# Optimization experiments

Hardware: AMD Instinct MI355X
Metric: run time of the kernel (lower is better)

The kernel has to match this reference:

```python
import jax, jax.numpy as jnp
import numpy as np

STATE_DIM = 256
ACTION_DIM = 2
HIDDEN = 512
N_HEADS = 5          # per ensemble; 2*N_HEADS stacked critics total
CEM_POP = 4096
CEM_ITERS = 4
ELITE_N = max(1, int(round(CEM_POP * 0.2)))  # 819
ACTION_LOW, ACTION_HIGH = -1.0, 1.0
INIT_STD, MIN_STD = 0.4, 0.1


def setup_inputs() -> dict:
    key = jax.random.key(0)
    ks = jax.random.split(key, 6)
    in_dim = STATE_DIM + ACTION_DIM
    state = jax.random.normal(ks[0], (1, STATE_DIM), dtype=jnp.float32)
    noise = jax.random.normal(ks[1], (CEM_ITERS, CEM_POP, ACTION_DIM), dtype=jnp.float32)
    W1 = jax.random.normal(ks[2], (2 * N_HEADS, in_dim, HIDDEN), dtype=jnp.float32) / np.sqrt(in_dim).astype(np.float32)
    b1 = jnp.zeros((2 * N_HEADS, HIDDEN), dtype=jnp.float32)
    W2 = jax.random.normal(ks[3], (2 * N_HEADS, HIDDEN, HIDDEN), dtype=jnp.float32) / np.sqrt(HIDDEN).astype(np.float32)
    b2 = jnp.zeros((2 * N_HEADS, HIDDEN), dtype=jnp.float32)
    W3 = jax.random.normal(ks[4], (2 * N_HEADS, HIDDEN, 1), dtype=jnp.float32) / np.sqrt(HIDDEN).astype(np.float32)
    b3 = jnp.zeros((2 * N_HEADS, 1), dtype=jnp.float32)
    return {"state": state, "noise": noise, "W1": W1, "b1": b1, "W2": W2, "b2": b2, "W3": W3, "b3": b3}


def _ensemble_scores(s_batch, a, W1, b1, W2, b2, W3, b3):
    # x: [P, state+action]; heads stacked on leading dim h = 2*N_HEADS
    x = jnp.concatenate([s_batch, a], axis=-1)
    h = jax.nn.relu(jnp.einsum('pi,hij->hpj', x, W1) + b1[:, None, :])
    h = jax.nn.relu(jnp.einsum('hpj,hjk->hpk', h, W2) + b2[:, None, :])
    q = (jnp.einsum('hpk,hko->hpo', h, W3) + b3[:, None, :])[..., 0]  # [2H, P]
    q1, q2 = q[:N_HEADS], q[N_HEADS:]
    return jnp.minimum(q1, q2).mean(axis=0)  # [P]


def reference(state, noise, W1, b1, W2, b2, W3, b3):
    s = state[0]  # squeeze(0)
    s_batch = jnp.broadcast_to(s, (CEM_POP, STATE_DIM))

    def step(carry, eps):
        mu, std, best_a, best_score = carry
        a = jnp.clip(mu + std * eps, ACTION_LOW, ACTION_HIGH)  # [P, A]
        scores = _ensemble_scores(s_batch, a, W1, b1, W2, b2, W3, b3)
        vals, idx = jax.lax.top_k(scores, ELITE_N)
        elite = a[idx]  # [ELITE_N, A]
        mu2 = elite.mean(axis=0)
        std2 = jnp.maximum(jnp.std(elite, axis=0, ddof=1), MIN_STD)  # torch unbiased std
        better = vals[0] > best_score
        best_a2 = jnp.where(better, elite[0], best_a)
        best_score2 = jnp.where(better, vals[0], best_score)
        return (mu2, std2, best_a2, best_score2), None

    carry0 = (jnp.zeros((ACTION_DIM,), jnp.float32),
              jnp.full((ACTION_DIM,), INIT_STD, jnp.float32),
              jnp.zeros((ACTION_DIM,), jnp.float32),
              jnp.float32(-jnp.inf))
    (mu, std, best_a, best_score), _ = jax.lax.scan(step, carry0, noise)
    return best_a[None, :]  # [1, ACTION_DIM]
```

## Files before the change

### kernel.cpp

```cpp
#include <hip/hip_runtime.h>
#include <math.h>

#define SDIM   256
#define HID    512
#define NH     5
#define HEADS  10
#define POP    4096
#define ITERS  4
#define ELITE  819
#define INIT_STDF 0.4f
#define MIN_STDF  0.1f

#define WS_BASE1 0
#define WS_Q     5120
#define WS_STATE 87040
#define WS_W2S_BYTE 348224
#define W2S_USHORTS (HEADS * 2 * 16 * 16384)
#define WS_NEED_BYTES (WS_W2S_BYTE + (size_t)W2S_USHORTS * 2)

typedef __attribute__((ext_vector_type(4))) float f32x4;
typedef __attribute__((ext_vector_type(8))) short bf16x8;

static __device__ __forceinline__ unsigned short bf16_rne(float x) {
    unsigned b = __float_as_uint(x);
    return (unsigned short)((b + 0x7FFFu + ((b >> 16) & 1u)) >> 16);
}

static __device__ __forceinline__ unsigned pack2(float x, float y) {
    unsigned r;
    asm("v_cvt_pk_bf16_f32 %0, %1, %2" : "=v"(r) : "v"(x), "v"(y));
    return r;
}

__global__ __launch_bounds__(256) void k_base(const float* __restrict__ state,
                                              const float* __restrict__ W1,
                                              const float* __restrict__ b1,
                                              float* __restrict__ ws)
{
    const int h = blockIdx.y;
    const int j = blockIdx.x * 256 + threadIdx.x;
    const float* w1h = W1 + (size_t)h * 258 * HID;
    float acc = b1[h * HID + j];
    for (int i = 0; i < SDIM; ++i)
        acc += state[i] * w1h[(size_t)i * HID + j];
    ws[WS_BASE1 + h * HID + j] = acc;

    if (h == 0 && blockIdx.x == 0 && threadIdx.x == 0) {
        float* st = ws + WS_STATE;
        st[0] = 0.f; st[1] = 0.f;
        st[2] = INIT_STDF; st[3] = INIT_STDF;
        st[4] = 0.f; st[5] = 0.f;
        st[6] = -3.402823466e38f;
    }
}

__global__ __launch_bounds__(256) void k_split(const float* __restrict__ W2,
                                               unsigned short* __restrict__ W2S)
{
    const int h = blockIdx.z, cb = blockIdx.y, jc = blockIdx.x;
    const int c = threadIdx.x;
    unsigned short* slab = W2S + (size_t)((h * 2 + cb) * 16 + jc) * 16384;
    #pragma unroll
    for (int jg = 0; jg < 4; ++jg) {
        unsigned hp[4], lp[4];
        #pragma unroll
        for (int i = 0; i < 4; ++i) {
            const int j = jc * 32 + jg * 8 + 2 * i;
            float v0 = W2[(size_t)(h * HID + j) * HID + cb * 256 + c];
            float v1 = W2[(size_t)(h * HID + j + 1) * HID + cb * 256 + c];
            unsigned short h0 = bf16_rne(v0), h1 = bf16_rne(v1);
            float f0 = __uint_as_float((unsigned)h0 << 16);
            float f1 = __uint_as_float((unsigned)h1 << 16);
            unsigned short l0 = bf16_rne(v0 - f0), l1 = bf16_rne(v1 - f1);
            hp[i] = (unsigned)h0 | ((unsigned)h1 << 16);
            lp[i] = (unsigned)l0 | ((unsigned)l1 << 16);
        }
        uint4 HV, LV;
        HV.x = hp[0]; HV.y = hp[1]; HV.z = hp[2]; HV.w = hp[3];
        LV.x = lp[0]; LV.y = lp[1]; LV.z = lp[2]; LV.w = lp[3];
        *(uint4*)&slab[jg * 2048 + c * 8] = HV;
        *(uint4*)&slab[8192 + jg * 2048 + c * 8] = LV;
    }
}

__global__ __launch_bounds__(256, 2) void k_score_mfma4(
    const float* __restrict__ noise, const float* __restrict__ W1,
    const unsigned short* __restrict__ W2S,
    const float* __restrict__ b2, const float* __restrict__ W3,
    float* __restrict__ ws, int t)
{
    __shared__ unsigned short As[2][8192];
    __shared__ float red[4][128];

    const int tid = threadIdx.x;
    const int bid = blockIdx.x;
    const int w = (bid & 7) * 80 + (bid >> 3);
    const int h = w >> 6;
    const int rem = w & 63;
    const int cb = rem >> 5;
    const int rb = rem & 31;

    const int lane = tid & 63;
    const int wc = tid >> 6;
    const int l15 = lane & 15, lk = lane >> 4;

    const int arow = tid & 127;
    const int khalf = tid >> 7;
    const float* st = ws + WS_STATE;
    float2 e = *(const float2*)&noise[((size_t)t * POP + rb * 128 + arow) * 2];
    const float a0 = fminf(fmaxf(st[0] + st[2] * e.x, -1.f), 1.f);
    const float a1 = fminf(fmaxf(st[1] + st[3] * e.y, -1.f), 1.f);

    const float* base1 = ws + WS_BASE1 + h * HID;
    const float* w1u = W1 + ((size_t)h * 258 + 256) * HID;
    const float* w1v = W1 + ((size_t)h * 258 + 257) * HID;
    const unsigned short* bslab = W2S + (size_t)((h * 2 + cb) * 16) * 16384;

    auto computeA = [&](int jc, int buf) {
        #pragma unroll
        for (int g = 0; g < 2; ++g) {
            const int j = jc * 32 + khalf * 16 + g * 8;
            f32x4 b0 = *(const f32x4*)&base1[j];
            f32x4 b1v = *(const f32x4*)&base1[j + 4];
            f32x4 u0 = *(const f32x4*)&w1u[j];
            f32x4 u1 = *(const f32x4*)&w1u[j + 4];
            f32x4 v0 = *(const f32x4*)&w1v[j];
            f32x4 v1 = *(const f32x4*)&w1v[j + 4];
            float hv[8];
            #pragma unroll
            for (int i = 0; i < 4; ++i) {
                hv[i]     = fmaxf(b0[i] + a0 * u0[i] + a1 * v0[i], 0.f);
                hv[4 + i] = fmaxf(b1v[i] + a0 * u1[i] + a1 * v1[i], 0.f);
            }
            unsigned ph[4], pl[4];
            #pragma unroll
            for (int i = 0; i < 4; ++i) {
                ph[i] = pack2(hv[2 * i], hv[2 * i + 1]);
                float fx = __uint_as_float(ph[i] << 16);
                float fy = __uint_as_float(ph[i] & 0xFFFF0000u);
                pl[i] = pack2(hv[2 * i] - fx, hv[2 * i + 1] - fy);
            }
            uint4 HV, LV;
            HV.x = ph[0]; HV.y = ph[1]; HV.z = ph[2]; HV.w = ph[3];
            LV.x = pl[0]; LV.y = pl[1]; LV.z = pl[2]; LV.w = pl[3];
            const int kg = khalf * 2 + g;
            *(uint4*)&As[buf][(kg * 128 + arow) * 8] = HV;
            *(uint4*)&As[buf][4096 + (kg * 128 + arow) * 8] = LV;
        }
    };

    const int bco = (wc * 64 + l15) * 8 + lk * 2048;

    f32x4 acc[8][4];
    #pragma unroll
    for (int m = 0; m < 8; ++m)
        #pragma unroll
        for (int n = 0; n < 4; ++n)
            acc[m][n] = (f32x4){0.f, 0.f, 0.f, 0.f};

    bf16x8 cBH[4], nBH[4], BL[4];
    computeA(0, 0);
    #pragma unroll
    for (int n = 0; n < 4; ++n)
        cBH[n] = *(const bf16x8*)(bslab + bco + n * 128);
    __syncthreads();

    for (int tt = 0; tt < 16; ++tt) {
        const int cur = tt & 1;
        const size_t chunk = (size_t)tt * 16384;
        #pragma unroll
        for (int n = 0; n < 4; ++n)
            BL[n] = *(const bf16x8*)(bslab + chunk + 8192 + bco + n * 128);
        if (tt < 15) {
            #pragma unroll
            for (int n = 0; n < 4; ++n)
                nBH[n] = *(const bf16x8*)(bslab + chunk + 16384 + bco + n * 128);
            computeA(tt + 1, cur ^ 1);
        }
        #pragma unroll
        for (int mg = 0; mg < 2; ++mg) {
            const int abase = (lk * 128 + mg * 64 + l15) * 8;
            bf16x8 AH[4], AL[4];
            #pragma unroll
            for (int m4 = 0; m4 < 4; ++m4) {
                AH[m4] = *(const bf16x8*)&As[cur][abase + m4 * 128];
                AL[m4] = *(const bf16x8*)&As[cur][4096 + abase + m4 * 128];
            }
            #pragma unroll
            for (int m4 = 0; m4 < 4; ++m4)
                #pragma unroll
                for (int n = 0; n < 4; ++n)
                    acc[mg * 4 + m4][n] = __builtin_amdgcn_mfma_f32_16x16x32_bf16(
                        AH[m4], cBH[n], acc[mg * 4 + m4][n], 0, 0, 0);
            #pragma unroll
            for (int m4 = 0; m4 < 4; ++m4)
                #pragma unroll
                for (int n = 0; n < 4; ++n)
                    acc[mg * 4 + m4][n] = __builtin_amdgcn_mfma_f32_16x16x32_bf16(
                        AL[m4], cBH[n], acc[mg * 4 + m4][n], 0, 0, 0);
            #pragma unroll
            for (int m4 = 0; m4 < 4; ++m4)
                #pragma unroll
                for (int n = 0; n < 4; ++n)
                    acc[mg * 4 + m4][n] = __builtin_amdgcn_mfma_f32_16x16x32_bf16(
                        AH[m4], BL[n], acc[mg * 4 + m4][n], 0, 0, 0);
        }
        __syncthreads();
        #pragma unroll
        for (int n = 0; n < 4; ++n) cBH[n] = nBH[n];
    }

    float qp[8][4];
    #pragma unroll
    for (int m = 0; m < 8; ++m)
        #pragma unroll
        for (int r = 0; r < 4; ++r) qp[m][r] = 0.f;
    #pragma unroll
    for (int n = 0; n < 4; ++n) {
        int gcol = cb * 256 + wc * 64 + n * 16 + l15;
        float b2v = b2[h * HID + gcol];
        float w3v = W3[h * HID + gcol];
        #pragma unroll
        for (int m = 0; m < 8; ++m)
            #pragma unroll
            for (int r = 0; r < 4; ++r)
                qp[m][r] += fmaxf(acc[m][n][r] + b2v, 0.f) * w3v;
    }
    #pragma unroll
    for (int m = 0; m < 8; ++m)
        #pragma unroll
        for (int r = 0; r < 4; ++r) {
            float v = qp[m][r];
            v += __shfl_xor(v, 1);
            v += __shfl_xor(v, 2);
            v += __shfl_xor(v, 4);
            v += __shfl_xor(v, 8);
            if (l15 == 0) red[wc][m * 16 + lk * 4 + r] = v;
        }
    __syncthreads();
    if (tid < 128) {
        float q = red[0][tid] + red[1][tid] + red[2][tid] + red[3][tid];
        ws[WS_Q + (size_t)(cb * HEADS + h) * POP + rb * 128 + tid] = q;
    }
}

__global__ __launch_bounds__(256) void k_score(const float* __restrict__ noise,
                                               const float* __restrict__ W1,
                                               const float* __restrict__ W2,
                                               const float* __restrict__ b2,
                                               const float* __restrict__ W3,
                                               float* __restrict__ ws, int t)
{
    __shared__ float h1[32][HID];
    __shared__ float a0s[32], a1s[32];
    __shared__ float red[2][16][2];

    const int tid = threadIdx.x;
    const int h   = blockIdx.y;
    const int p0  = blockIdx.x * 32;

    if (tid < 32) {
        const float* st = ws + WS_STATE;
        const int p = p0 + tid;
        float e0 = noise[((size_t)t * POP + p) * 2 + 0];
        float e1 = noise[((size_t)t * POP + p) * 2 + 1];
        a0s[tid] = fminf(fmaxf(st[0] + st[2] * e0, -1.f), 1.f);
        a1s[tid] = fminf(fmaxf(st[1] + st[3] * e1, -1.f), 1.f);
    }
    __syncthreads();

    const float* base1 = ws + WS_BASE1 + h * HID;
    const float* w1u = W1 + ((size_t)h * 258 + 256) * HID;
    const float* w1v = W1 + ((size_t)h * 258 + 257) * HID;
    #pragma unroll
    for (int jj = 0; jj < 2; ++jj) {
        int j = tid + jj * 256;
        float bb = base1[j], uu = w1u[j], vv = w1v[j];
        #pragma unroll
        for (int p = 0; p < 32; ++p)
            h1[p][j] = fmaxf(bb + a0s[p] * uu + a1s[p] * vv, 0.f);
    }
    __syncthreads();

    const int pg = tid >> 7;
    const int kl = tid & 127;
    const float* W2h = W2 + (size_t)h * HID * HID + kl;

    float acc[16][4];
    #pragma unroll
    for (int p = 0; p < 16; ++p)
        #pragma unroll
        for (int dk = 0; dk < 4; ++dk) acc[p][dk] = 0.f;

    for (int j0 = 0; j0 < HID; j0 += 4) {
        float w[4][4];
        #pragma unroll
        for (int dj = 0; dj < 4; ++dj)
            #pragma unroll
            for (int dk = 0; dk < 4; ++dk)
                w[dj][dk] = W2h[(size_t)(j0 + dj) * HID + dk * 128];
        #pragma unroll
        for (int p = 0; p < 16; ++p) {
            const float4 hv = *(const float4*)&h1[pg * 16 + p][j0];
            #pragma unroll
            for (int dk = 0; dk < 4; ++dk)
                acc[p][dk] += hv.x * w[0][dk] + hv.y * w[1][dk]
                            + hv.z * w[2][dk] + hv.w * w[3][dk];
        }
    }

    float b2v[4], w3v[4];
    #pragma unroll
    for (int dk = 0; dk < 4; ++dk) {
        b2v[dk] = b2[h * HID + kl + dk * 128];
        w3v[dk] = W3[h * HID + kl + dk * 128];
    }
    const int wid  = tid >> 6;
    const int lane = tid & 63;
    const int wig  = wid & 1;
    #pragma unroll
    for (int p = 0; p < 16; ++p) {
        float v = 0.f;
        #pragma unroll
        for (int dk = 0; dk < 4; ++dk)
            v += fmaxf(acc[p][dk] + b2v[dk], 0.f) * w3v[dk];
        #pragma unroll
        for (int off = 32; off; off >>= 1) v += __shfl_down(v, off);
        if (lane == 0) red[pg][p][wig] = v;
    }
    __syncthreads();
    if (tid < 32) {
        int pp = tid & 15, g = tid >> 4;
        ws[WS_Q + (size_t)h * POP + p0 + g * 16 + pp] =
            red[g][pp][0] + red[g][pp][1];
        ws[WS_Q + (size_t)(HEADS + h) * POP + p0 + g * 16 + pp] = 0.f;
    }
}

__global__ __launch_bounds__(256) void k_select(const float* __restrict__ noise,
                                                const float* __restrict__ b3,
                                                float* __restrict__ ws,
                                                float* __restrict__ out, int t)
{
    __shared__ float    sc[POP];
    __shared__ unsigned uk[POP];
    __shared__ unsigned hist[256];
    __shared__ int      scan[256];
    __shared__ float    rf[256];
    __shared__ int      ri_[256];
    __shared__ double   rd[256];
    __shared__ unsigned s_prefix;
    __shared__ int      s_r;

    const int tid = threadIdx.x;
    const float* q = ws + WS_Q;
    float* st = ws + WS_STATE;
    const float mu0 = st[0], mu1 = st[1], sd0 = st[2], sd1 = st[3];

    #pragma unroll
    for (int g = 0; g < 4; ++g) {
        const int p = g * 1024 + tid * 4;
        f32x4 s = (f32x4){0.f, 0.f, 0.f, 0.f};
        #pragma unroll
        for (int hh = 0; hh < NH; ++hh) {
            f32x4 qa0 = *(const f32x4*)&q[(size_t)hh * POP + p];
            f32x4 qa1 = *(const f32x4*)&q[(size_t)(HEADS + hh) * POP + p];
            f32x4 qb0 = *(const f32x4*)&q[(size_t)(NH + hh) * POP + p];
            f32x4 qb1 = *(const f32x4*)&q[(size_t)(HEADS + NH + hh) * POP + p];
            float ba = b3[hh], bb = b3[NH + hh];
            #pragma unroll
            for (int i = 0; i < 4; ++i)
                s[i] += fminf(qa0[i] + qa1[i] + ba, qb0[i] + qb1[i] + bb);
        }
        #pragma unroll
        for (int i = 0; i < 4; ++i) {
            float v = s[i] * 0.2f;
            sc[p + i] = v;
            unsigned b = __float_as_uint(v);
            uk[p + i] = (b & 0x80000000u) ? ~b : (b | 0x80000000u);
        }
    }
    __syncthreads();

    float mv = -3.402823466e38f; int mi = 0;
    for (int p = tid; p < POP; p += 256) {
        float v = sc[p];
        if (v > mv) { mv = v; mi = p; }
    }
    rf[tid] = mv; ri_[tid] = mi;
    __syncthreads();
    for (int off = 128; off; off >>= 1) {
        if (tid < off) {
            float ov = rf[tid + off]; int oi = ri_[tid + off];
            if (ov > rf[tid] || (ov == rf[tid] && oi < ri_[tid])) {
                rf[tid] = ov; ri_[tid] = oi;
            }
        }
        __syncthreads();
    }
    const float maxsc = rf[0];
    const int argmax = ri_[0];
    __syncthreads();

    unsigned prefix = 0; int r = ELITE;
    for (int shift = 24; shift >= 0; shift -= 8) {
        hist[tid] = 0;
        __syncthreads();
        const unsigned himask = (shift < 24) ? (0xFFFFFFFFu << (shift + 8)) : 0u;
        for (int p = tid; p < POP; p += 256) {
            unsigned key = uk[p];
            if ((key & himask) == prefix)
                atomicAdd(&hist[(key >> shift) & 255u], 1u);
        }
        __syncthreads();
        scan[tid] = (int)hist[tid];
        __syncthreads();
        for (int off = 1; off < 256; off <<= 1) {
            int v = (tid + off < 256) ? scan[tid + off] : 0;
            __syncthreads();
            scan[tid] += v;
            __syncthreads();
        }
        int above = (tid < 255) ? scan[tid + 1] : 0;
        if (scan[tid] >= r && above < r) {
            s_prefix = prefix | ((unsigned)tid << shift);
            s_r = r - above;
        }
        __syncthreads();
        prefix = s_prefix; r = s_r;
        __syncthreads();
    }
    const unsigned uT = prefix;
    const int take = r;

    int tieloc = 0;
    {
        const int base = tid * 16;
        #pragma unroll
        for (int k = 0; k < 16; ++k) if (uk[base + k] == uT) tieloc++;
    }
    scan[tid] = tieloc;
    __syncthreads();
    for (int off = 1; off < 256; off <<= 1) {
        int v = (tid >= off) ? scan[tid - off] : 0;
        __syncthreads();
        scan[tid] += v;
        __syncthreads();
    }
    const int tieExcl = scan[tid] - tieloc;

    double s0 = 0, s1 = 0, ss0 = 0, ss1 = 0;
    {
        const int base = tid * 16;
        int trank = tieExcl;
        for (int k = 0; k < 16; ++k) {
            const int p = base + k;
            const unsigned key = uk[p];
            bool inc = false;
            if (key > uT) inc = true;
            else if (key == uT) { if (trank < take) inc = true; trank++; }
            if (inc) {
                float e0 = noise[((size_t)t * POP + p) * 2 + 0];
                float e1 = noise[((size_t)t * POP + p) * 2 + 1];
                float a0 = fminf(fmaxf(mu0 + sd0 * e0, -1.f), 1.f);
                float a1 = fminf(fmaxf(mu1 + sd1 * e1, -1.f), 1.f);
                s0 += a0; s1 += a1;
                ss0 += (double)a0 * a0; ss1 += (double)a1 * a1;
            }
        }
    }
    double S0, S1, SS0, SS1;
    rd[tid] = s0;  __syncthreads();
    for (int off = 128; off; off >>= 1) { if (tid < off) rd[tid] += rd[tid + off]; __syncthreads(); }
    S0 = rd[0]; __syncthreads();
    rd[tid] = s1;  __syncthreads();
    for (int off = 128; off; off >>= 1) { if (tid < off) rd[tid] += rd[tid + off]; __syncthreads(); }
    S1 = rd[0]; __syncthreads();
    rd[tid] = ss0; __syncthreads();
    for (int off = 128; off; off >>= 1) { if (tid < off) rd[tid] += rd[tid + off]; __syncthreads(); }
    SS0 = rd[0]; __syncthreads();
    rd[tid] = ss1; __syncthreads();
    for (int off = 128; off; off >>= 1) { if (tid < off) rd[tid] += rd[tid + off]; __syncthreads(); }
    SS1 = rd[0]; __syncthreads();

    if (tid == 0) {
        const double n = (double)ELITE;
        double m0 = S0 / n, m1 = S1 / n;
        double v0 = (SS0 - S0 * S0 / n) / (n - 1.0);
        double v1 = (SS1 - S1 * S1 / n) / (n - 1.0);
        float nsd0 = fmaxf((float)sqrt(fmax(v0, 0.0)), MIN_STDF);
        float nsd1 = fmaxf((float)sqrt(fmax(v1, 0.0)), MIN_STDF);
        float e0 = noise[((size_t)t * POP + argmax) * 2 + 0];
        float e1 = noise[((size_t)t * POP + argmax) * 2 + 1];
        float a0 = fminf(fmaxf(mu0 + sd0 * e0, -1.f), 1.f);
        float a1 = fminf(fmaxf(mu1 + sd1 * e1, -1.f), 1.f);
        if (maxsc > st[6]) { st[4] = a0; st[5] = a1; st[6] = maxsc; }
        st[0] = (float)m0; st[1] = (float)m1; st[2] = nsd0; st[3] = nsd1;
        if (t == ITERS - 1) { out[0] = st[4]; out[1] = st[5]; }
    }
}

extern "C" void kernel_launch(void* const* d_in, const int* in_sizes, int n_in,
                              void* d_out, int out_size, void* d_ws, size_t ws_size,
                              hipStream_t stream)
{
    const float* state = (const float*)d_in[0];
    const float* noise = (const float*)d_in[1];
    const float* W1    = (const float*)d_in[2];
    const float* b1    = (const float*)d_in[3];
    const float* W2    = (const float*)d_in[4];
    const float* b2    = (const float*)d_in[5];
    const float* W3    = (const float*)d_in[6];
    const float* b3    = (const float*)d_in[7];
    float* out = (float*)d_out;
    float* ws  = (float*)d_ws;

    const bool fast = ws_size >= WS_NEED_BYTES;

    k_base<<<dim3(2, HEADS), 256, 0, stream>>>(state, W1, b1, ws);
    if (fast) {
        unsigned short* W2S = (unsigned short*)((char*)d_ws + WS_W2S_BYTE);
        k_split<<<dim3(16, 2, HEADS), 256, 0, stream>>>(W2, W2S);
        for (int t = 0; t < ITERS; ++t) {
            k_score_mfma4<<<dim3(640), 256, 0, stream>>>(
                noise, W1, W2S, b2, W3, ws, t);
            k_select<<<1, 256, 0, stream>>>(noise, b3, ws, out, t);
        }
    } else {
        for (int t = 0; t < ITERS; ++t) {
            k_score<<<dim3(POP / 32, HEADS), 256, 0, stream>>>(noise, W1, W2, b2, W3, ws, t);
            k_select<<<1, 256, 0, stream>>>(noise, b3, ws, out, t);
        }
    }
}
```

Measured before the change: 368.9 us.

## Build layer-1 activations in registers, drop LDS staging, halve row tile

The score kernel no longer stages layer-1 hidden activations in shared memory. Each wave computes its own A fragments (hi and lo bf16 split) directly in registers, so the per-chunk __syncthreads is removed. The row tile per block drops from 128 to 64, which doubles the grid to 1280 blocks and halves the accumulator registers. Layer-1 weight vectors are prefetched one chunk ahead, and s_setprio raises priority around the MFMA bursts. The cost is that all four waves now compute the same A fragments redundantly, and each B fragment is reused over half as many rows, which doubles B traffic from L2.

After: 400.6 us. 8.6% more time.

```diff
diff --git a/kernel.cpp b/kernel.cpp
--- a/kernel.cpp
+++ b/kernel.cpp
@@ -30,6 +30,17 @@
     unsigned r;
     asm("v_cvt_pk_bf16_f32 %0, %1, %2" : "=v"(r) : "v"(x), "v"(y));
     return r;
+}
+
+static __device__ __forceinline__ bf16x8 mk8(unsigned p0, unsigned p1,
+                                             unsigned p2, unsigned p3) {
+    union { unsigned u[4]; bf16x8 v; } c;
+    c.u[0] = p0; c.u[1] = p1; c.u[2] = p2; c.u[3] = p3;
+    return c.v;
+}
+
+static __device__ __forceinline__ float clip1(float x) {
+    return fminf(fmaxf(x, -1.f), 1.f);
 }
 
 __global__ __launch_bounds__(256) void k_base(const float* __restrict__ state,
@@ -83,54 +94,88 @@
     }
 }
 
-__global__ __launch_bounds__(256, 2) void k_score_mfma4(
+__global__ __launch_bounds__(256, 2) void k_score_mfma5(
     const float* __restrict__ noise, const float* __restrict__ W1,
     const unsigned short* __restrict__ W2S,
     const float* __restrict__ b2, const float* __restrict__ W3,
     float* __restrict__ ws, int t)
 {
-    __shared__ unsigned short As[2][8192];
-    __shared__ float red[4][128];
+    __shared__ float red[4][64];
 
     const int tid = threadIdx.x;
     const int bid = blockIdx.x;
-    const int w = (bid & 7) * 80 + (bid >> 3);
-    const int h = w >> 6;
-    const int rem = w & 63;
-    const int cb = rem >> 5;
-    const int rb = rem & 31;
+    const int w = (bid & 7) * 160 + (bid >> 3);
+    const int h = w >> 7;
+    const int rem = w & 127;
+    const int cb = rem >> 6;
+    const int rs = rem & 63;
 
     const int lane = tid & 63;
-    const int wc = tid >> 6;
+    const int wv = tid >> 6;
     const int l15 = lane & 15, lk = lane >> 4;
 
-    const int arow = tid & 127;
-    const int khalf = tid >> 7;
     const float* st = ws + WS_STATE;
-    float2 e = *(const float2*)&noise[((size_t)t * POP + rb * 128 + arow) * 2];
-    const float a0 = fminf(fmaxf(st[0] + st[2] * e.x, -1.f), 1.f);
-    const float a1 = fminf(fmaxf(st[1] + st[3] * e.y, -1.f), 1.f);
+    const float mu0 = st[0], mu1 = st[1], sd0 = st[2], sd1 = st[3];
+    float a0[4], a1[4];
+    #pragma unroll
+    for (int m = 0; m < 4; ++m) {
+        int r = rs * 64 + m * 16 + l15;
+        float2 e = *(const float2*)&noise[((size_t)t * POP + r) * 2];
+        a0[m] = clip1(mu0 + sd0 * e.x);
+        a1[m] = clip1(mu1 + sd1 * e.y);
+    }
 
     const float* base1 = ws + WS_BASE1 + h * HID;
     const float* w1u = W1 + ((size_t)h * 258 + 256) * HID;
     const float* w1v = W1 + ((size_t)h * 258 + 257) * HID;
     const unsigned short* bslab = W2S + (size_t)((h * 2 + cb) * 16) * 16384;
-
-    auto computeA = [&](int jc, int buf) {
-        #pragma unroll
-        for (int g = 0; g < 2; ++g) {
-            const int j = jc * 32 + khalf * 16 + g * 8;
-            f32x4 b0 = *(const f32x4*)&base1[j];
-            f32x4 b1v = *(const f32x4*)&base1[j + 4];
-            f32x4 u0 = *(const f32x4*)&w1u[j];
-            f32x4 u1 = *(const f32x4*)&w1u[j + 4];
-            f32x4 v0 = *(const f32x4*)&w1v[j];
-            f32x4 v1 = *(const f32x4*)&w1v[j + 4];
+    const int bco = lk * 2048 + (wv * 64 + l15) * 8;
+
+    f32x4 acc[4][4];
+    #pragma unroll
+    for (int m = 0; m < 4; ++m)
+        #pragma unroll
+        for (int n = 0; n < 4; ++n)
+            acc[m][n] = (f32x4){0.f, 0.f, 0.f, 0.f};
+
+    f32x4 pb0 = *(const f32x4*)&base1[lk * 8];
+    f32x4 pb1 = *(const f32x4*)&base1[lk * 8 + 4];
+    f32x4 pu0 = *(const f32x4*)&w1u[lk * 8];
+    f32x4 pu1 = *(const f32x4*)&w1u[lk * 8 + 4];
+    f32x4 pv0 = *(const f32x4*)&w1v[lk * 8];
+    f32x4 pv1 = *(const f32x4*)&w1v[lk * 8 + 4];
+    bf16x8 BH[4];
+    #pragma unroll
+    for (int n = 0; n < 4; ++n)
+        BH[n] = *(const bf16x8*)(bslab + bco + n * 128);
+
+    for (int kc = 0; kc < 16; ++kc) {
+        const size_t ch = (size_t)kc * 16384;
+        bf16x8 BL[4], nBH[4];
+        #pragma unroll
+        for (int n = 0; n < 4; ++n)
+            BL[n] = *(const bf16x8*)(bslab + ch + 8192 + bco + n * 128);
+        f32x4 qb0, qb1, qu0, qu1, qv0, qv1;
+        if (kc < 15) {
+            #pragma unroll
+            for (int n = 0; n < 4; ++n)
+                nBH[n] = *(const bf16x8*)(bslab + ch + 16384 + bco + n * 128);
+            const int j = (kc + 1) * 32 + lk * 8;
+            qb0 = *(const f32x4*)&base1[j];
+            qb1 = *(const f32x4*)&base1[j + 4];
+            qu0 = *(const f32x4*)&w1u[j];
+            qu1 = *(const f32x4*)&w1u[j + 4];
+            qv0 = *(const f32x4*)&w1v[j];
+            qv1 = *(const f32x4*)&w1v[j + 4];
+        }
+        bf16x8 AH[4], AL[4];
+        #pragma unroll
+        for (int m = 0; m < 4; ++m) {
             float hv[8];
             #pragma unroll
             for (int i = 0; i < 4; ++i) {
-                hv[i]     = fmaxf(b0[i] + a0 * u0[i] + a1 * v0[i], 0.f);
-                hv[4 + i] = fmaxf(b1v[i] + a0 * u1[i] + a1 * v1[i], 0.f);
+                hv[i]     = fmaxf(pb0[i] + a0[m] * pu0[i] + a1[m] * pv0[i], 0.f);
+                hv[4 + i] = fmaxf(pb1[i] + a0[m] * pu1[i] + a1[m] * pv1[i], 0.f);
             }
             unsigned ph[4], pl[4];
             #pragma unroll
@@ -140,94 +185,56 @@
                 float fy = __uint_as_float(ph[i] & 0xFFFF0000u);
                 pl[i] = pack2(hv[2 * i] - fx, hv[2 * i + 1] - fy);
             }
-            uint4 HV, LV;
-            HV.x = ph[0]; HV.y = ph[1]; HV.z = ph[2]; HV.w = ph[3];
-            LV.x = pl[0]; LV.y = pl[1]; LV.z = pl[2]; LV.w = pl[3];
-            const int kg = khalf * 2 + g;
-            *(uint4*)&As[buf][(kg * 128 + arow) * 8] = HV;
-            *(uint4*)&As[buf][4096 + (kg * 128 + arow) * 8] = LV;
-        }
-    };
-
-    const int bco = (wc * 64 + l15) * 8 + lk * 2048;
-
-    f32x4 acc[8][4];
-    #pragma unroll
-    for (int m = 0; m < 8; ++m)
-        #pragma unroll
-        for (int n = 0; n < 4; ++n)
-            acc[m][n] = (f32x4){0.f, 0.f, 0.f, 0.f};
-
-    bf16x8 cBH[4], nBH[4], BL[4];
-    computeA(0, 0);
-    #pragma unroll
-    for (int n = 0; n < 4; ++n)
-        cBH[n] = *(const bf16x8*)(bslab + bco + n * 128);
-    __syncthreads();
-
-    for (int tt = 0; tt < 16; ++tt) {
-        const int cur = tt & 1;
-        const size_t chunk = (size_t)tt * 16384;
-        #pragma unroll
-        for (int n = 0; n < 4; ++n)
-            BL[n] = *(const bf16x8*)(bslab + chunk + 8192 + bco + n * 128);
-        if (tt < 15) {
+            AH[m] = mk8(ph[0], ph[1], ph[2], ph[3]);
+            AL[m] = mk8(pl[0], pl[1], pl[2], pl[3]);
+        }
+        __builtin_amdgcn_s_setprio(1);
+        #pragma unroll
+        for (int m = 0; m < 4; ++m)
             #pragma unroll
             for (int n = 0; n < 4; ++n)
-                nBH[n] = *(const bf16x8*)(bslab + chunk + 16384 + bco + n * 128);
-            computeA(tt + 1, cur ^ 1);
-        }
-        #pragma unroll
-        for (int mg = 0; mg < 2; ++mg) {
-            const int abase = (lk * 128 + mg * 64 + l15) * 8;
-            bf16x8 AH[4], AL[4];
-            #pragma unroll
-            for (int m4 = 0; m4 < 4; ++m4) {
-                AH[m4] = *(const bf16x8*)&As[cur][abase + m4 * 128];
-                AL[m4] = *(const bf16x8*)&As[cur][4096 + abase + m4 * 128];
-            }
-            #pragma unroll
-            for (int m4 = 0; m4 < 4; ++m4)
-                #pragma unroll
-                for (int n = 0; n < 4; ++n)
-                    acc[mg * 4 + m4][n] = __builtin_amdgcn_mfma_f32_16x16x32_bf16(
-                        AH[m4], cBH[n], acc[mg * 4 + m4][n], 0, 0, 0);
-            #pragma unroll
-            for (int m4 = 0; m4 < 4; ++m4)
-                #pragma unroll
-                for (int n = 0; n < 4; ++n)
-                    acc[mg * 4 + m4][n] = __builtin_amdgcn_mfma_f32_16x16x32_bf16(
-                        AL[m4], cBH[n], acc[mg * 4 + m4][n], 0, 0, 0);
-            #pragma unroll
-            for (int m4 = 0; m4 < 4; ++m4)
-                #pragma unroll
-                for (int n = 0; n < 4; ++n)
-                    acc[mg * 4 + m4][n] = __builtin_amdgcn_mfma_f32_16x16x32_bf16(
-                        AH[m4], BL[n], acc[mg * 4 + m4][n], 0, 0, 0);
-        }
-        __syncthreads();
-        #pragma unroll
-        for (int n = 0; n < 4; ++n) cBH[n] = nBH[n];
-    }
-
-    float qp[8][4];
-    #pragma unroll
-    for (int m = 0; m < 8; ++m)
+                acc[m][n] = __builtin_amdgcn_mfma_f32_16x16x32_bf16(
+                    AH[m], BH[n], acc[m][n], 0, 0, 0);
+        #pragma unroll
+        for (int m = 0; m < 4; ++m)
+            #pragma unroll
+            for (int n = 0; n < 4; ++n)
+                acc[m][n] = __builtin_amdgcn_mfma_f32_16x16x32_bf16(
+                    AL[m], BH[n], acc[m][n], 0, 0, 0);
+        #pragma unroll
+        for (int m = 0; m < 4; ++m)
+            #pragma unroll
+            for (int n = 0; n < 4; ++n)
+                acc[m][n] = __builtin_amdgcn_mfma_f32_16x16x32_bf16(
+                    AH[m], BL[n], acc[m][n], 0, 0, 0);
+        __builtin_amdgcn_s_setprio(0);
+        if (kc < 15) {
+            #pragma unroll
+            for (int n = 0; n < 4; ++n) BH[n] = nBH[n];
+            pb0 = qb0; pb1 = qb1;
+            pu0 = qu0; pu1 = qu1;
+            pv0 = qv0; pv1 = qv1;
+        }
+    }
+
+    float qp[4][4];
+    #pragma unroll
+    for (int m = 0; m < 4; ++m)
         #pragma unroll
         for (int r = 0; r < 4; ++r) qp[m][r] = 0.f;
     #pragma unroll
     for (int n = 0; n < 4; ++n) {
-        int gcol = cb * 256 + wc * 64 + n * 16 + l15;
+        int gcol = cb * 256 + wv * 64 + n * 16 + l15;
         float b2v = b2[h * HID + gcol];
         float w3v = W3[h * HID + gcol];
         #pragma unroll
-        for (int m = 0; m < 8; ++m)
+        for (int m = 0; m < 4; ++m)
             #pragma unroll
             for (int r = 0; r < 4; ++r)
                 qp[m][r] += fmaxf(acc[m][n][r] + b2v, 0.f) * w3v;
     }
     #pragma unroll
-    for (int m = 0; m < 8; ++m)
+    for (int m = 0; m < 4; ++m)
         #pragma unroll
         for (int r = 0; r < 4; ++r) {
             float v = qp[m][r];
@@ -235,12 +242,12 @@
             v += __shfl_xor(v, 2);
             v += __shfl_xor(v, 4);
             v += __shfl_xor(v, 8);
-            if (l15 == 0) red[wc][m * 16 + lk * 4 + r] = v;
-        }
-    __syncthreads();
-    if (tid < 128) {
+            if (l15 == 0) red[wv][m * 16 + lk * 4 + r] = v;
+        }
+    __syncthreads();
+    if (tid < 64) {
         float q = red[0][tid] + red[1][tid] + red[2][tid] + red[3][tid];
-        ws[WS_Q + (size_t)(cb * HEADS + h) * POP + rb * 128 + tid] = q;
+        ws[WS_Q + (size_t)(cb * HEADS + h) * POP + rs * 64 + tid] = q;
     }
 }
 
@@ -522,7 +529,7 @@
         unsigned short* W2S = (unsigned short*)((char*)d_ws + WS_W2S_BYTE);
         k_split<<<dim3(16, 2, HEADS), 256, 0, stream>>>(W2, W2S);
         for (int t = 0; t < ITERS; ++t) {
-            k_score_mfma4<<<dim3(640), 256, 0, stream>>>(
+            k_score_mfma5<<<dim3(1280), 256, 0, stream>>>(
                 noise, W1, W2S, b2, W3, ws, t);
             k_select<<<1, 256, 0, stream>>>(noise, b3, ws, out, t);
         }
```
